# Kernel tuning notes

Hardware: AMD Instinct MI355X
Metric: run time of the kernel (lower is better)

## Reference

```python
import jax, jax.numpy as jnp
import numpy as np

N_NODES = 50000
N_EDGES = 800000
IN_DIM = 128
HID_DIM = 128
OUT_DIM = 128
NUM_GRAPHS = 64
NUM_CLASSES = 3


def _glorot(key, shape):
    lim = np.sqrt(6.0 / (shape[0] + shape[1])).astype(np.float32)
    return jax.random.uniform(key, shape, jnp.float32, -lim, lim)


def setup_inputs() -> dict:
    key = jax.random.key(0)
    ks = jax.random.split(key, 10)
    x = jax.random.normal(ks[0], (N_NODES, IN_DIM), jnp.float32)
    edge_index = jax.random.randint(ks[1], (2, N_EDGES), 0, N_NODES, jnp.int32).astype(jnp.int64)
    batch = jnp.sort(jax.random.randint(ks[2], (N_NODES,), 0, NUM_GRAPHS, jnp.int32)).astype(jnp.int64)
    return {
        "x": x,
        "edge_index": edge_index,
        "batch": batch,
        "W1": _glorot(ks[3], (IN_DIM, HID_DIM)),  "b1": jnp.zeros((HID_DIM,), jnp.float32),
        "W2": _glorot(ks[4], (HID_DIM, HID_DIM)), "b2": jnp.zeros((HID_DIM,), jnp.float32),
        "W3": _glorot(ks[5], (HID_DIM, OUT_DIM)), "b3": jnp.zeros((OUT_DIM,), jnp.float32),
        "C1": _glorot(ks[6], (OUT_DIM, HID_DIM)), "bc1": jnp.zeros((HID_DIM,), jnp.float32),
        "C2": _glorot(ks[7], (HID_DIM, NUM_CLASSES)), "bc2": jnp.zeros((NUM_CLASSES,), jnp.float32),
    }


def _gcn_conv(x, src, dst, norm, W, b):
    # PyG GCNConv: linear transform, then normalized gather/scatter aggregation, then bias.
    h = x @ W                               # [N, F_out]
    msg = h[src] * norm[:, None]            # [E+N, F_out] irregular gather
    return jax.ops.segment_sum(msg, dst, num_segments=N_NODES) + b


def reference(x, edge_index, batch, W1, b1, W2, b2, W3, b3, C1, bc1, C2, bc2):
    loops = jnp.arange(N_NODES, dtype=edge_index.dtype)
    src = jnp.concatenate([edge_index[0], loops])  # add self-loops as in GCNConv
    dst = jnp.concatenate([edge_index[1], loops])
    deg = jax.ops.segment_sum(jnp.ones_like(dst, jnp.float32), dst, num_segments=N_NODES)
    dinv = jnp.where(deg > 0, jax.lax.rsqrt(deg), 0.0)
    norm = dinv[src] * dinv[dst]            # symmetric D^-1/2 (A+I) D^-1/2 weights

    # dropout(p=0.2) is identity at inference time
    h = jax.nn.relu(_gcn_conv(x, src, dst, norm, W1, b1))
    h = jax.nn.relu(_gcn_conv(h, src, dst, norm, W2, b2))
    h = _gcn_conv(h, src, dst, norm, W3, b3)

    # global mean pool over batch segment ids
    counts = jax.ops.segment_sum(jnp.ones((N_NODES,), jnp.float32), batch, num_segments=NUM_GRAPHS)
    pooled = jax.ops.segment_sum(h, batch, num_segments=NUM_GRAPHS) / jnp.maximum(counts, 1.0)[:, None]

    g = jax.nn.relu(pooled @ C1 + bc1)      # classifier MLP (dropout 0.3 inactive)
    return g @ C2 + bc2                     # [NUM_GRAPHS, 3]
```

## Files before the change

### kernel.cpp

```cpp
#include <hip/hip_runtime.h>
#include <hip/hip_bf16.h>

#define N_NODES    50000
#define DIM        128
#define NUM_GRAPHS 64
#define NUM_CLASSES 3
#define NPAD       50176
#define XPITCH     136

typedef unsigned short ushort_t;
typedef unsigned int   uint_t;
typedef __attribute__((ext_vector_type(8))) short short8;
typedef __attribute__((ext_vector_type(4))) float f32x4;

__device__ __forceinline__ ushort_t f2bf(float f) {
    union { float f; uint_t u; } v; v.f = f;
    uint_t r = v.u + 0x7fffu + ((v.u >> 16) & 1u);
    return (ushort_t)(r >> 16);
}
__device__ __forceinline__ float bflo(uint_t u) {
    union { uint_t u; float f; } v; v.u = u << 16; return v.f;
}
__device__ __forceinline__ float bfhi(uint_t u) {
    union { uint_t u; float f; } v; v.u = u & 0xffff0000u; return v.f;
}

__device__ __forceinline__ void gather_row(
    int n, int lane, const int* __restrict__ rowptr,
    const int* __restrict__ csr_src, const float* __restrict__ dinv,
    const uint_t* __restrict__ Tb, float2& acc)
{
    int p0 = rowptr[n], p1 = rowptr[n + 1];
    float dd = dinv[n];
    uint_t us = Tb[n * 64 + lane];
    float sl = dd * dd;
    acc.x += bflo(us) * sl; acc.y += bfhi(us) * sl;
    int p = p0;
    for (; p + 8 <= p1; p += 8) {
        int s[8]; uint_t u[8]; float w[8];
        #pragma unroll
        for (int q = 0; q < 8; ++q) s[q] = csr_src[p + q];
        #pragma unroll
        for (int q = 0; q < 8; ++q) u[q] = Tb[s[q] * 64 + lane];
        #pragma unroll
        for (int q = 0; q < 8; ++q) w[q] = dinv[s[q]] * dd;
        #pragma unroll
        for (int q = 0; q < 8; ++q) {
            acc.x += bflo(u[q]) * w[q];
            acc.y += bfhi(u[q]) * w[q];
        }
    }
    for (; p + 4 <= p1; p += 4) {
        int s[4]; uint_t u[4]; float w[4];
        #pragma unroll
        for (int q = 0; q < 4; ++q) s[q] = csr_src[p + q];
        #pragma unroll
        for (int q = 0; q < 4; ++q) u[q] = Tb[s[q] * 64 + lane];
        #pragma unroll
        for (int q = 0; q < 4; ++q) w[q] = dinv[s[q]] * dd;
        #pragma unroll
        for (int q = 0; q < 4; ++q) {
            acc.x += bflo(u[q]) * w[q];
            acc.y += bfhi(u[q]) * w[q];
        }
    }
    for (; p < p1; ++p) {
        int s = csr_src[p];
        uint_t u = Tb[s * 64 + lane];
        float w = dinv[s] * dd;
        acc.x += bflo(u) * w; acc.y += bfhi(u) * w;
    }
}

__global__ void k_init(int* degi, float* pooled, float* counts) {
    int i = blockIdx.x * 256 + threadIdx.x;
    if (i < NPAD) degi[i] = 0;
    if (i < NUM_GRAPHS * DIM) pooled[i] = 0.0f;
    if (i < NUM_GRAPHS) counts[i] = 0.0f;
}

__global__ void k_prep(const float* __restrict__ W1, const float* __restrict__ W2,
                       const float* __restrict__ W3, ushort_t* __restrict__ Wt) {
    int i = blockIdx.x * 256 + threadIdx.x;
    int mat = i >> 14;
    int idx = i & 16383;
    const float* W = (mat == 0) ? W1 : (mat == 1) ? W2 : W3;
    int n = idx >> 7, k = idx & 127;
    Wt[mat * 16384 + n * 128 + k] = f2bf(W[k * 128 + n]);
}

__global__ void k_count(const int* __restrict__ dst, int* degi, int* rank, int nedges) {
    int e = blockIdx.x * 256 + threadIdx.x;
    if (e < nedges) rank[e] = atomicAdd(&degi[dst[e]], 1);
}

__global__ __launch_bounds__(256) void k_scan1(const int* __restrict__ degi,
                                               int* rowptr, int* bsum) {
    __shared__ int sh[256];
    int i = blockIdx.x * 256 + threadIdx.x;
    int v = degi[i];
    sh[threadIdx.x] = v;
    __syncthreads();
    for (int off = 1; off < 256; off <<= 1) {
        int t = (threadIdx.x >= off) ? sh[threadIdx.x - off] : 0;
        __syncthreads();
        sh[threadIdx.x] += t;
        __syncthreads();
    }
    rowptr[i] = sh[threadIdx.x] - v;
    if (threadIdx.x == 255) bsum[blockIdx.x] = sh[255];
}

__global__ __launch_bounds__(256) void k_scan2(int* bsum, int nblocks) {
    __shared__ int sh[256];
    int v = (threadIdx.x < nblocks) ? bsum[threadIdx.x] : 0;
    sh[threadIdx.x] = v;
    __syncthreads();
    for (int off = 1; off < 256; off <<= 1) {
        int t = (threadIdx.x >= off) ? sh[threadIdx.x - off] : 0;
        __syncthreads();
        sh[threadIdx.x] += t;
        __syncthreads();
    }
    if (threadIdx.x < nblocks) bsum[threadIdx.x] = sh[threadIdx.x] - v;
}

__global__ __launch_bounds__(256) void k_scan3(int* rowptr, const int* __restrict__ bsum,
                                               const int* __restrict__ degi,
                                               float* dinv) {
    int i = blockIdx.x * 256 + threadIdx.x;
    rowptr[i] = rowptr[i] + bsum[blockIdx.x];
    if (i < N_NODES) dinv[i] = rsqrtf((float)degi[i] + 1.0f);
}

__global__ void k_fill(const int* __restrict__ src, const int* __restrict__ dst,
                       const int* __restrict__ rank, const int* __restrict__ rowptr,
                       int* csr_src, int nedges) {
    int e = blockIdx.x * 256 + threadIdx.x;
    if (e < nedges) csr_src[rowptr[dst[e]] + rank[e]] = src[e];
}

__global__ __launch_bounds__(256) void k_mm1(
    const float* __restrict__ xin, const ushort_t* __restrict__ WtG,
    ushort_t* __restrict__ TbOut)
{
    __shared__ ushort_t Wl[DIM * XPITCH];
    __shared__ ushort_t Xl[64 * XPITCH];

    const int tid = threadIdx.x;
    const int rowbase = blockIdx.x * 64;

    #pragma unroll
    for (int i = 0; i < 8; ++i) {
        int g = tid + i * 256;
        uint4 v = ((const uint4*)WtG)[g];
        *((uint4*)&Wl[(g >> 4) * XPITCH + (g & 15) * 8]) = v;
    }
    #pragma unroll
    for (int i = 0; i < 8; ++i) {
        int c = tid + i * 256;
        int row = c >> 5;
        int grow = rowbase + row;
        float4 f = make_float4(0.f, 0.f, 0.f, 0.f);
        if (grow < N_NODES)
            f = ((const float4*)xin)[(long long)rowbase * 32 + c];
        ushort4 h;
        h.x = f2bf(f.x); h.y = f2bf(f.y); h.z = f2bf(f.z); h.w = f2bf(f.w);
        *((ushort4*)&Xl[row * XPITCH + (c & 31) * 4]) = h;
    }
    __syncthreads();

    const int wave = tid >> 6;
    const int lane = tid & 63;
    const int quad = lane >> 4;
    const int lm   = lane & 15;
    const int m0   = wave * 16;

    short8 af[4];
    #pragma unroll
    for (int k0 = 0; k0 < 4; ++k0)
        af[k0] = *(const short8*)&Xl[(m0 + lm) * XPITCH + k0 * 32 + quad * 8];

    for (int n0 = 0; n0 < DIM; n0 += 16) {
        f32x4 acc = {0.f, 0.f, 0.f, 0.f};
        #pragma unroll
        for (int k0 = 0; k0 < 4; ++k0) {
            short8 bf = *(const short8*)&Wl[(n0 + lm) * XPITCH + k0 * 32 + quad * 8];
            acc = __builtin_amdgcn_mfma_f32_16x16x32_bf16(af[k0], bf, acc, 0, 0, 0);
        }
        int n = n0 + lm;
        #pragma unroll
        for (int r = 0; r < 4; ++r) {
            int node = rowbase + m0 + quad * 4 + r;
            if (node < N_NODES)
                TbOut[(long long)node * DIM + n] = f2bf(acc[r]);
        }
    }
}

__global__ __launch_bounds__(256) void k_fused(
    const int* __restrict__ rowptr, const int* __restrict__ csr_src,
    const float* __restrict__ dinv, const uint_t* __restrict__ TbIn,
    const ushort_t* __restrict__ WtG, const float* __restrict__ b_prev,
    ushort_t* __restrict__ TbOut)
{
    __shared__ ushort_t Xl[16 * XPITCH];

    const int tid = threadIdx.x;
    const int rowbase = blockIdx.x * 16;
    const int wave = tid >> 6;
    const int lane = tid & 63;

    float2 bias2 = ((const float2*)b_prev)[lane];

    #pragma unroll
    for (int t = 0; t < 4; ++t) {
        int r = wave * 4 + t;
        int n = rowbase + r;
        float2 acc = bias2;
        if (n < N_NODES) {
            gather_row(n, lane, rowptr, csr_src, dinv, TbIn, acc);
        } else {
            acc.x = 0.f; acc.y = 0.f;
        }
        ushort2 h;
        h.x = f2bf(fmaxf(acc.x, 0.f));
        h.y = f2bf(fmaxf(acc.y, 0.f));
        *((ushort2*)&Xl[r * XPITCH + lane * 2]) = h;
    }
    __syncthreads();

    const int quad = lane >> 4;
    const int lm   = lane & 15;

    short8 af[4];
    #pragma unroll
    for (int k0 = 0; k0 < 4; ++k0)
        af[k0] = *(const short8*)&Xl[lm * XPITCH + k0 * 32 + quad * 8];

    #pragma unroll
    for (int h = 0; h < 2; ++h) {
        int n0 = wave * 32 + h * 16;
        f32x4 acc = {0.f, 0.f, 0.f, 0.f};
        #pragma unroll
        for (int k0 = 0; k0 < 4; ++k0) {
            short8 bf = *(const short8*)&WtG[(n0 + lm) * DIM + k0 * 32 + quad * 8];
            acc = __builtin_amdgcn_mfma_f32_16x16x32_bf16(af[k0], bf, acc, 0, 0, 0);
        }
        int n = n0 + lm;
        #pragma unroll
        for (int r = 0; r < 4; ++r) {
            int node = rowbase + quad * 4 + r;
            if (node < N_NODES)
                TbOut[(long long)node * DIM + n] = f2bf(acc[r]);
        }
    }
}

__global__ __launch_bounds__(256) void k_poolgather(
    const int* __restrict__ rowptr, const int* __restrict__ csr_src,
    const float* __restrict__ dinv, const uint_t* __restrict__ Tb,
    const float* __restrict__ b3, const int* __restrict__ batch,
    float* pooled, float* counts)
{
    const int wave = threadIdx.x >> 6;
    const int lane = threadIdx.x & 63;
    int n0 = blockIdx.x * 32 + wave * 8;
    if (n0 >= N_NODES) return;
    int nend = min(n0 + 8, N_NODES);

    float2 bias2 = ((const float2*)b3)[lane];
    int cur = batch[n0];
    int runstart = n0;
    float2 pacc = make_float2(0.f, 0.f);

    for (int n = n0; n < nend; ++n) {
        int g = batch[n];
        if (g != cur) {
            atomicAdd(&pooled[cur * DIM + 2 * lane], pacc.x);
            atomicAdd(&pooled[cur * DIM + 2 * lane + 1], pacc.y);
            if (lane == 0) atomicAdd(&counts[cur], (float)(n - runstart));
            pacc.x = 0.f; pacc.y = 0.f; cur = g; runstart = n;
        }
        float2 h = bias2;
        gather_row(n, lane, rowptr, csr_src, dinv, Tb, h);
        pacc.x += h.x; pacc.y += h.y;
    }
    atomicAdd(&pooled[cur * DIM + 2 * lane], pacc.x);
    atomicAdd(&pooled[cur * DIM + 2 * lane + 1], pacc.y);
    if (lane == 0) atomicAdd(&counts[cur], (float)(nend - runstart));
}

__global__ __launch_bounds__(128) void k_cls(
    const float* __restrict__ pooled, const float* __restrict__ counts,
    const float* __restrict__ C1, const float* __restrict__ bc1,
    const float* __restrict__ C2, const float* __restrict__ bc2,
    float* out)
{
    __shared__ float pm[DIM];
    __shared__ float gv[DIM];
    int g = blockIdx.x, j = threadIdx.x;
    float cnt = fmaxf(counts[g], 1.0f);
    pm[j] = pooled[g * DIM + j] / cnt;
    __syncthreads();
    float a = bc1[j];
    for (int k = 0; k < DIM; ++k) a += pm[k] * C1[k * DIM + j];
    gv[j] = fmaxf(a, 0.f);
    __syncthreads();
    if (j < NUM_CLASSES) {
        float o = bc2[j];
        for (int k = 0; k < DIM; ++k) o += gv[k] * C2[k * NUM_CLASSES + j];
        out[g * NUM_CLASSES + j] = o;
    }
}

extern "C" void kernel_launch(void* const* d_in, const int* in_sizes, int n_in,
                              void* d_out, int out_size, void* d_ws, size_t ws_size,
                              hipStream_t stream) {
    const float* x    = (const float*)d_in[0];
    const int*   ei   = (const int*)d_in[1];
    const int*   batch= (const int*)d_in[2];
    const float* W1   = (const float*)d_in[3];
    const float* b1   = (const float*)d_in[4];
    const float* W2   = (const float*)d_in[5];
    const float* b2   = (const float*)d_in[6];
    const float* W3   = (const float*)d_in[7];
    const float* b3   = (const float*)d_in[8];
    const float* C1   = (const float*)d_in[9];
    const float* bc1  = (const float*)d_in[10];
    const float* C2   = (const float*)d_in[11];
    const float* bc2  = (const float*)d_in[12];

    const int nedges = in_sizes[1] / 2;
    const int* src = ei;
    const int* dst = ei + nedges;

    float*    dinv    = (float*)d_ws;
    uint_t*   TbA     = (uint_t*)(dinv + NPAD);
    uint_t*   TbB     = TbA + (long long)N_NODES * 64;
    float*    pooled  = (float*)(TbB + (long long)N_NODES * 64);
    float*    counts  = pooled + NUM_GRAPHS * DIM;
    int*      degi    = (int*)(counts + 64);
    int*      rowptr  = degi + NPAD;
    int*      bsum    = rowptr + NPAD + 256;
    int*      rank    = bsum + 256;
    int*      csr_src = rank + nedges;
    ushort_t* Wt      = (ushort_t*)(csr_src + nedges);

    const int nodeBlocks = NPAD / 256;
    const int mmBlocks   = (N_NODES + 63) / 64;
    const int fusedBlocks= (N_NODES + 15) / 16;
    const int pgBlocks   = (N_NODES + 31) / 32;
    const int edgeBlocks = (nedges + 255) / 256;

    k_init<<<nodeBlocks, 256, 0, stream>>>(degi, pooled, counts);
    k_prep<<<192, 256, 0, stream>>>(W1, W2, W3, Wt);
    k_count<<<edgeBlocks, 256, 0, stream>>>(dst, degi, rank, nedges);
    k_scan1<<<nodeBlocks, 256, 0, stream>>>(degi, rowptr, bsum);
    k_scan2<<<1, 256, 0, stream>>>(bsum, nodeBlocks);
    k_scan3<<<nodeBlocks, 256, 0, stream>>>(rowptr, bsum, degi, dinv);
    k_fill<<<edgeBlocks, 256, 0, stream>>>(src, dst, rank, rowptr, csr_src, nedges);

    k_mm1<<<mmBlocks, 256, 0, stream>>>(x, Wt, (ushort_t*)TbA);
    k_fused<<<fusedBlocks, 256, 0, stream>>>(rowptr, csr_src, dinv, TbA,
                                             Wt + 16384, b1, (ushort_t*)TbB);
    k_fused<<<fusedBlocks, 256, 0, stream>>>(rowptr, csr_src, dinv, TbB,
                                             Wt + 32768, b2, (ushort_t*)TbA);
    k_poolgather<<<pgBlocks, 256, 0, stream>>>(rowptr, csr_src, dinv, TbA,
                                               b3, batch, pooled, counts);
    k_cls<<<NUM_GRAPHS, 128, 0, stream>>>(pooled, counts, C1, bc1, C2, bc2,
                                          (float*)d_out);
}
```

Measured before the change: 336.2 us.

## Fold symmetric normalization into matmul epilogues to drop per-edge dinv gathers

Pre-scales each transformed row by dinv[src] in the matmul epilogue and applies dinv[dst] once per destination row after aggregation. The inner gather loop then does no per-edge dinv lookup and no multiply, leaving one irregular load stream instead of two. The gather loop also gets a 16-wide unroll with two accumulators, and the pooling gather kernel handles 4 nodes per wave instead of 8 for more parallelism. Storing the pre-scaled features in bf16 slightly changes rounding.

```diff
diff --git a/kernel.cpp b/kernel.cpp
--- a/kernel.cpp
+++ b/kernel.cpp
@@ -25,51 +25,59 @@
     union { uint_t u; float f; } v; v.u = u & 0xffff0000u; return v.f;
 }
 
-__device__ __forceinline__ void gather_row(
+__device__ __forceinline__ void gather_raw(
     int n, int lane, const int* __restrict__ rowptr,
-    const int* __restrict__ csr_src, const float* __restrict__ dinv,
-    const uint_t* __restrict__ Tb, float2& acc)
+    const int* __restrict__ csr_src, const uint_t* __restrict__ Tb,
+    float2& acc)
 {
     int p0 = rowptr[n], p1 = rowptr[n + 1];
-    float dd = dinv[n];
     uint_t us = Tb[n * 64 + lane];
-    float sl = dd * dd;
-    acc.x += bflo(us) * sl; acc.y += bfhi(us) * sl;
+    float2 a0 = make_float2(bflo(us), bfhi(us));
+    float2 a1 = make_float2(0.f, 0.f);
     int p = p0;
+    for (; p + 16 <= p1; p += 16) {
+        int s[16]; uint_t u[16];
+        #pragma unroll
+        for (int q = 0; q < 16; ++q) s[q] = csr_src[p + q];
+        #pragma unroll
+        for (int q = 0; q < 16; ++q) u[q] = Tb[s[q] * 64 + lane];
+        #pragma unroll
+        for (int q = 0; q < 16; q += 2) {
+            a0.x += bflo(u[q]);     a0.y += bfhi(u[q]);
+            a1.x += bflo(u[q + 1]); a1.y += bfhi(u[q + 1]);
+        }
+    }
     for (; p + 8 <= p1; p += 8) {
-        int s[8]; uint_t u[8]; float w[8];
+        int s[8]; uint_t u[8];
         #pragma unroll
         for (int q = 0; q < 8; ++q) s[q] = csr_src[p + q];
         #pragma unroll
         for (int q = 0; q < 8; ++q) u[q] = Tb[s[q] * 64 + lane];
         #pragma unroll
-        for (int q = 0; q < 8; ++q) w[q] = dinv[s[q]] * dd;
-        #pragma unroll
-        for (int q = 0; q < 8; ++q) {
-            acc.x += bflo(u[q]) * w[q];
-            acc.y += bfhi(u[q]) * w[q];
+        for (int q = 0; q < 8; q += 2) {
+            a0.x += bflo(u[q]);     a0.y += bfhi(u[q]);
+            a1.x += bflo(u[q + 1]); a1.y += bfhi(u[q + 1]);
         }
     }
     for (; p + 4 <= p1; p += 4) {
-        int s[4]; uint_t u[4]; float w[4];
+        int s[4]; uint_t u[4];
         #pragma unroll
         for (int q = 0; q < 4; ++q) s[q] = csr_src[p + q];
         #pragma unroll
         for (int q = 0; q < 4; ++q) u[q] = Tb[s[q] * 64 + lane];
         #pragma unroll
-        for (int q = 0; q < 4; ++q) w[q] = dinv[s[q]] * dd;
-        #pragma unroll
-        for (int q = 0; q < 4; ++q) {
-            acc.x += bflo(u[q]) * w[q];
-            acc.y += bfhi(u[q]) * w[q];
+        for (int q = 0; q < 4; q += 2) {
+            a0.x += bflo(u[q]);     a0.y += bfhi(u[q]);
+            a1.x += bflo(u[q + 1]); a1.y += bfhi(u[q + 1]);
         }
     }
     for (; p < p1; ++p) {
         int s = csr_src[p];
         uint_t u = Tb[s * 64 + lane];
-        float w = dinv[s] * dd;
-        acc.x += bflo(u) * w; acc.y += bfhi(u) * w;
-    }
+        a0.x += bflo(u); a0.y += bfhi(u);
+    }
+    acc.x += a0.x + a1.x;
+    acc.y += a0.y + a1.y;
 }
 
 __global__ void k_init(int* degi, float* pooled, float* counts) {
@@ -142,7 +150,7 @@
 
 __global__ __launch_bounds__(256) void k_mm1(
     const float* __restrict__ xin, const ushort_t* __restrict__ WtG,
-    ushort_t* __restrict__ TbOut)
+    const float* __restrict__ dinv, ushort_t* __restrict__ TbOut)
 {
     __shared__ ushort_t Wl[DIM * XPITCH];
     __shared__ ushort_t Xl[64 * XPITCH];
@@ -181,6 +189,14 @@
     for (int k0 = 0; k0 < 4; ++k0)
         af[k0] = *(const short8*)&Xl[(m0 + lm) * XPITCH + k0 * 32 + quad * 8];
 
+    int noder[4]; float di[4]; bool okr[4];
+    #pragma unroll
+    for (int r = 0; r < 4; ++r) {
+        noder[r] = rowbase + m0 + quad * 4 + r;
+        okr[r] = (noder[r] < N_NODES);
+        di[r] = okr[r] ? dinv[noder[r]] : 0.f;
+    }
+
     for (int n0 = 0; n0 < DIM; n0 += 16) {
         f32x4 acc = {0.f, 0.f, 0.f, 0.f};
         #pragma unroll
@@ -190,11 +206,9 @@
         }
         int n = n0 + lm;
         #pragma unroll
-        for (int r = 0; r < 4; ++r) {
-            int node = rowbase + m0 + quad * 4 + r;
-            if (node < N_NODES)
-                TbOut[(long long)node * DIM + n] = f2bf(acc[r]);
-        }
+        for (int r = 0; r < 4; ++r)
+            if (okr[r])
+                TbOut[(long long)noder[r] * DIM + n] = f2bf(acc[r] * di[r]);
     }
 }
 
@@ -217,15 +231,15 @@
     for (int t = 0; t < 4; ++t) {
         int r = wave * 4 + t;
         int n = rowbase + r;
-        float2 acc = bias2;
+        float2 acc = make_float2(0.f, 0.f);
+        float dd = 0.f;
         if (n < N_NODES) {
-            gather_row(n, lane, rowptr, csr_src, dinv, TbIn, acc);
-        } else {
-            acc.x = 0.f; acc.y = 0.f;
+            dd = dinv[n];
+            gather_raw(n, lane, rowptr, csr_src, TbIn, acc);
         }
         ushort2 h;
-        h.x = f2bf(fmaxf(acc.x, 0.f));
-        h.y = f2bf(fmaxf(acc.y, 0.f));
+        h.x = f2bf(fmaxf(bias2.x + acc.x * dd, 0.f));
+        h.y = f2bf(fmaxf(bias2.y + acc.y * dd, 0.f));
         *((ushort2*)&Xl[r * XPITCH + lane * 2]) = h;
     }
     __syncthreads();
@@ -237,6 +251,14 @@
     #pragma unroll
     for (int k0 = 0; k0 < 4; ++k0)
         af[k0] = *(const short8*)&Xl[lm * XPITCH + k0 * 32 + quad * 8];
+
+    int noder[4]; float di[4]; bool okr[4];
+    #pragma unroll
+    for (int r = 0; r < 4; ++r) {
+        noder[r] = rowbase + quad * 4 + r;
+        okr[r] = (noder[r] < N_NODES);
+        di[r] = okr[r] ? dinv[noder[r]] : 0.f;
+    }
 
     #pragma unroll
     for (int h = 0; h < 2; ++h) {
@@ -249,11 +271,9 @@
         }
         int n = n0 + lm;
         #pragma unroll
-        for (int r = 0; r < 4; ++r) {
-            int node = rowbase + quad * 4 + r;
-            if (node < N_NODES)
-                TbOut[(long long)node * DIM + n] = f2bf(acc[r]);
-        }
+        for (int r = 0; r < 4; ++r)
+            if (okr[r])
+                TbOut[(long long)noder[r] * DIM + n] = f2bf(acc[r] * di[r]);
     }
 }
 
@@ -265,9 +285,9 @@
 {
     const int wave = threadIdx.x >> 6;
     const int lane = threadIdx.x & 63;
-    int n0 = blockIdx.x * 32 + wave * 8;
+    int n0 = blockIdx.x * 16 + wave * 4;
     if (n0 >= N_NODES) return;
-    int nend = min(n0 + 8, N_NODES);
+    int nend = min(n0 + 4, N_NODES);
 
     float2 bias2 = ((const float2*)b3)[lane];
     int cur = batch[n0];
@@ -282,9 +302,11 @@
             if (lane == 0) atomicAdd(&counts[cur], (float)(n - runstart));
             pacc.x = 0.f; pacc.y = 0.f; cur = g; runstart = n;
         }
-        float2 h = bias2;
-        gather_row(n, lane, rowptr, csr_src, dinv, Tb, h);
-        pacc.x += h.x; pacc.y += h.y;
+        float2 acc = make_float2(0.f, 0.f);
+        gather_raw(n, lane, rowptr, csr_src, Tb, acc);
+        float dd = dinv[n];
+        pacc.x += bias2.x + acc.x * dd;
+        pacc.y += bias2.y + acc.y * dd;
     }
     atomicAdd(&pooled[cur * DIM + 2 * lane], pacc.x);
     atomicAdd(&pooled[cur * DIM + 2 * lane + 1], pacc.y);
@@ -350,7 +372,6 @@
     const int nodeBlocks = NPAD / 256;
     const int mmBlocks   = (N_NODES + 63) / 64;
     const int fusedBlocks= (N_NODES + 15) / 16;
-    const int pgBlocks   = (N_NODES + 31) / 32;
     const int edgeBlocks = (nedges + 255) / 256;
 
     k_init<<<nodeBlocks, 256, 0, stream>>>(degi, pooled, counts);
@@ -361,13 +382,13 @@
     k_scan3<<<nodeBlocks, 256, 0, stream>>>(rowptr, bsum, degi, dinv);
     k_fill<<<edgeBlocks, 256, 0, stream>>>(src, dst, rank, rowptr, csr_src, nedges);
 
-    k_mm1<<<mmBlocks, 256, 0, stream>>>(x, Wt, (ushort_t*)TbA);
+    k_mm1<<<mmBlocks, 256, 0, stream>>>(x, Wt, dinv, (ushort_t*)TbA);
     k_fused<<<fusedBlocks, 256, 0, stream>>>(rowptr, csr_src, dinv, TbA,
                                              Wt + 16384, b1, (ushort_t*)TbB);
     k_fused<<<fusedBlocks, 256, 0, stream>>>(rowptr, csr_src, dinv, TbB,
                                              Wt + 32768, b2, (ushort_t*)TbA);
-    k_poolgather<<<pgBlocks, 256, 0, stream>>>(rowptr, csr_src, dinv, TbA,
-                                               b3, batch, pooled, counts);
+    k_poolgather<<<fusedBlocks, 256, 0, stream>>>(rowptr, csr_src, dinv, TbA,
+                                                  b3, batch, pooled, counts);
     k_cls<<<NUM_GRAPHS, 128, 0, stream>>>(pooled, counts, C1, bc1, C2, bc2,
                                           (float*)d_out);
 }
```

Result: slower. 370.6 us (+10.2%).
